# Performance work log

Measured on AMD Instinct MI355X. Metric: run time of the kernel, lower is better.

The kernel has to match this reference:

```python
import jax, jax.numpy as jnp
import numpy as np
from jax import lax

RATIOS = (0.5, 1.0, 2.0)
SCALES = (8, 16, 32)
BASE = 16
STRIDE = 16
N_PRE = 6000
N_POST = 300      # post-NMS proposals kept
NMS_THRESH = 0.7
MIN_SIZE = 16.0


def _anchor_base():
    x = y = BASE / 2.0
    ab = np.zeros((len(RATIOS) * len(SCALES), 4), np.float32)
    for i, r in enumerate(RATIOS):
        for j, s in enumerate(SCALES):
            h = BASE * s * np.sqrt(r)
            w = BASE * s * np.sqrt(1.0 / r)
            k = i * len(SCALES) + j
            ab[k] = [y - h / 2, x - w / 2, y + h / 2, x + w / 2]
    return ab


def _anchors(h, w):
    ab = _anchor_base()
    sy = np.arange(0, h * STRIDE, STRIDE)
    sx = np.arange(0, w * STRIDE, STRIDE)
    sx, sy = np.meshgrid(sx, sy)
    shift = np.stack((sy.ravel(), sx.ravel(), sy.ravel(), sx.ravel()), axis=1)
    # [K, A, 4] -> [K*A, 4], row-major over (y, x) pixels matching NHWC flatten
    return (ab[None, :, :] + shift[:, None, :]).reshape(-1, 4).astype(np.float32)


def _conv(x, w, b, pad):
    y = lax.conv_general_dilated(x, w, (1, 1), ((pad, pad), (pad, pad)),
                                 dimension_numbers=('NCHW', 'OIHW', 'NCHW'))
    return y + b[None, :, None, None]


def _loc2bbox(anchor, loc):
    h = anchor[:, 2] - anchor[:, 0]
    w = anchor[:, 3] - anchor[:, 1]
    cy = anchor[:, 0] + 0.5 * h
    cx = anchor[:, 1] + 0.5 * w
    dy, dx, dh, dw = loc[:, 0], loc[:, 1], loc[:, 2], loc[:, 3]
    ncy = dy * h + cy
    ncx = dx * w + cx
    nh = jnp.exp(dh) * h
    nw = jnp.exp(dw) * w
    return jnp.stack([ncy - 0.5 * nh, ncx - 0.5 * nw, ncy + 0.5 * nh, ncx + 0.5 * nw], axis=1)


def _iou(b):
    tl = jnp.maximum(b[:, None, :2], b[None, :, :2])
    br = jnp.minimum(b[:, None, 2:], b[None, :, 2:])
    wh = jnp.clip(br - tl, 0.0)
    inter = wh[..., 0] * wh[..., 1]
    area = (b[:, 2] - b[:, 0]) * (b[:, 3] - b[:, 1])
    return inter / (area[:, None] + area[None, :] - inter + 1e-9)


def _nms_keep(iou):
    # greedy NMS over score-sorted boxes: suppress later boxes overlapping kept earlier ones
    n = iou.shape[0]
    idx = jnp.arange(n)
    def step(keep, i):
        sup = (iou[i] > NMS_THRESH) & (idx > i) & keep[i]
        return keep & (~sup), None
    keep, _ = lax.scan(step, jnp.ones((n,), dtype=bool), idx)
    return keep


def _proposal(loc, fg, anchor, img_h, img_w, scale=1.0):
    boxes = _loc2bbox(anchor, loc)
    boxes = jnp.stack([jnp.clip(boxes[:, 0], 0.0, img_h),
                       jnp.clip(boxes[:, 1], 0.0, img_w),
                       jnp.clip(boxes[:, 2], 0.0, img_h),
                       jnp.clip(boxes[:, 3], 0.0, img_w)], axis=1)
    hs = boxes[:, 2] - boxes[:, 0]
    ws = boxes[:, 3] - boxes[:, 1]
    ms = MIN_SIZE * scale
    score = jnp.where((hs >= ms) & (ws >= ms), fg, -jnp.inf)
    top, idx = lax.top_k(score, N_PRE)
    bk = boxes[idx]                                    # [N_PRE, 4]
    keep = _nms_keep(_iou(lax.stop_gradient(bk)))      # selection is non-differentiable
    fs = jnp.where(keep, top, -jnp.inf)
    _, o2 = lax.top_k(fs, N_POST)
    return bk[o2]                                      # [N_POST, 4]


def setup_inputs() -> dict:
    key = jax.random.key(0)
    ks = jax.random.split(key, 4)
    C, H, W = 512, 50, 76
    return {
        "feature": jax.random.normal(ks[0], (1, C, H, W), jnp.float32),
        "conv1_w": jax.random.normal(ks[1], (512, C, 3, 3), jnp.float32) * 0.01,
        "conv1_b": jnp.zeros((512,), jnp.float32),
        "score_w": jax.random.normal(ks[2], (18, 512, 1, 1), jnp.float32) * 0.01,
        "score_b": jnp.zeros((18,), jnp.float32),
        "loc_w": jax.random.normal(ks[3], (36, 512, 1, 1), jnp.float32) * 0.01,
        "loc_b": jnp.zeros((36,), jnp.float32),
        "img_h": 800,
        "img_w": 1216,
    }


def reference(feature, conv1_w, conv1_b, score_w, score_b, loc_w, loc_b, img_h, img_w):
    _, c, h, w = feature.shape
    A = 9
    anchor = jnp.asarray(_anchors(h, w))
    x = jax.nn.relu(_conv(feature, conv1_w, conv1_b, 1))
    locs = _conv(x, loc_w, loc_b, 0)
    rpn_locs = locs.transpose(0, 2, 3, 1).reshape(1, -1, 4)
    sc = _conv(x, score_w, score_b, 0).transpose(0, 2, 3, 1)   # [1, h, w, 2A]
    sm = jax.nn.softmax(sc.reshape(1, h, w, A, 2), axis=-1)
    fg = sm[..., 1].reshape(-1)
    rpn_scores = sc.reshape(1, -1, 2)
    rois = _proposal(rpn_locs[0], fg, anchor, float(img_h), float(img_w), scale=1.0)
    return rpn_locs, rpn_scores, rois, anchor
```

## Files before the change

### kernel.cpp

```cpp
#include <hip/hip_runtime.h>

#define HH 50
#define WW2 76
#define NPIX 3800
#define CIN 512
#define NANCH 34200
#define NPRE 6000
#define NPOST 300
#define WPR 94

typedef unsigned long long u64;
typedef unsigned int u32;

__device__ __forceinline__ int PADL(int i) { return i + (i >> 4); }

template <bool DOW>
__global__ __launch_bounds__(256) void rpn_wtrans(const float* __restrict__ wgt,
                                                  float* __restrict__ wt,
                                                  const float* __restrict__ sw,
                                                  const float* __restrict__ lw,
                                                  float* __restrict__ wt2,
                                                  u32* __restrict__ hist,
                                                  u32* __restrict__ info) {
    __shared__ float tile[32][33];
    const int bx = blockIdx.x;
    const int by = blockIdx.y;
    const int t  = threadIdx.x;
    const int tx = t & 31, ty = t >> 5;
    int gid = (by * 144 + bx) * 256 + t;
    if (gid < 65536) hist[gid] = 0u;
    else if (gid < 65552) info[gid - 65536] = 0u;
    if (gid < 32768) {
        int c = gid >> 6, n = gid & 63;
        float v = 0.f;
        if (n < 18) v = sw[n * 512 + c];
        else if (n < 54) v = lw[(n - 18) * 512 + c];
        wt2[((c >> 2) * 64 + n) * 4 + (c & 3)] = v;
    }
    if (!DOW) return;
#pragma unroll
    for (int r = 0; r < 32; r += 8) {
        int ko = by * 32 + ty + r;
        tile[ty + r][tx] = wgt[(size_t)ko * 4608 + bx * 32 + tx];
    }
    __syncthreads();
#pragma unroll
    for (int r = 0; r < 32; r += 8) {
        int cit = bx * 32 + ty + r;
        wt[(size_t)cit * 512 + by * 32 + tx] = tile[tx][ty + r];
    }
}

template <bool USEWT>
__global__ __launch_bounds__(256, 4) void rpn_conv1(
    const float* __restrict__ feat, const float* __restrict__ wsrc,
    float* __restrict__ Xp, int cin_blk) {
    const int yb = blockIdx.x;
    const int kg = blockIdx.y;
    const int cz = blockIdx.z;
    const int t  = threadIdx.x;
    const int kp = t & 31;
    const int ty = t >> 5;
    const int row  = ty >> 2;
    const int xseg = ty & 3;
    const int x0 = xseg * 20;
    __shared__ float in_l[2816];
    __shared__ float w_l[4608];

    const int y0 = yb * 2 - 1;
    int inSrc[11]; u32 inValid = 0, inPad = 0;
#pragma unroll
    for (int k = 0; k < 11; ++k) {
        int q = t + k * 256;
        int c = q / 336, rem = q - c * 336;
        int r = rem / 84, xx = rem - r * 84;
        int gy = y0 + r, gx = xx - 1;
        bool inb = q < 2688;
        bool ok = inb && ((unsigned)gy < 50u) && ((unsigned)gx < 76u);
        inSrc[k] = c * NPIX + gy * 76 + gx;
        if (ok) inValid |= (1u << k);
        else if (inb) inPad |= (1u << k);
    }
#pragma unroll
    for (int k = 0; k < 11; ++k)
        if ((inPad >> k) & 1) in_l[t + k * 256] = 0.f;

    const float* wb;
    int wOffA = 0;
    int wSrc[18];
    if (USEWT) {
        wb = wsrc + (size_t)(cz * cin_blk) * 9 * 512 + kg * 64;
        wOffA = 8 * t - 7 * (t & 63);
    } else {
        wb = wsrc + (size_t)(kg * 64) * 4608 + (size_t)(cz * cin_blk) * 9;
#pragma unroll
        for (int k = 0; k < 18; ++k) {
            int q = t + k * 256;
            int c = q / 576, r2 = q - c * 576;
            int tap = r2 >> 6, ko = r2 & 63;
            wSrc[k] = ko * 4608 + c * 9 + tap;
        }
    }

    const float* fb = feat + (size_t)(cz * cin_blk) * NPIX;
    float acc0[20], acc1[20];
#pragma unroll
    for (int p = 0; p < 20; ++p) { acc0[p] = 0.f; acc1[p] = 0.f; }

    const int niter = cin_blk >> 3;
#pragma unroll 1
    for (int it = 0; it < niter; ++it) {
        __syncthreads();
#pragma unroll
        for (int k = 0; k < 11; ++k)
            if ((inValid >> k) & 1) in_l[t + k * 256] = fb[inSrc[k]];
        if (USEWT) {
#pragma unroll
            for (int k = 0; k < 18; ++k)
                w_l[t + k * 256] = wb[wOffA + k * 2048];
        } else {
#pragma unroll
            for (int k = 0; k < 18; ++k)
                w_l[t + k * 256] = wb[wSrc[k]];
        }
        __syncthreads();
#pragma unroll 1
        for (int c = 0; c < 8; ++c) {
            const float* ir0 = &in_l[(c * 4 + row) * 84 + x0];
            const float* wl  = &w_l[c * 576 + 2 * kp];
#pragma unroll
            for (int r = 0; r < 3; ++r) {
                const float* ir = ir0 + r * 84;
                float win[22];
#pragma unroll
                for (int w = 0; w < 22; ++w) win[w] = ir[w];
                float w00 = wl[(r * 3 + 0) * 64],     w01 = wl[(r * 3 + 1) * 64],     w02 = wl[(r * 3 + 2) * 64];
                float w10 = wl[(r * 3 + 0) * 64 + 1], w11 = wl[(r * 3 + 1) * 64 + 1], w12 = wl[(r * 3 + 2) * 64 + 1];
#pragma unroll
                for (int p = 0; p < 20; ++p) {
                    acc0[p] = fmaf(w00, win[p],     acc0[p]);
                    acc0[p] = fmaf(w01, win[p + 1], acc0[p]);
                    acc0[p] = fmaf(w02, win[p + 2], acc0[p]);
                    acc1[p] = fmaf(w10, win[p],     acc1[p]);
                    acc1[p] = fmaf(w11, win[p + 1], acc1[p]);
                    acc1[p] = fmaf(w12, win[p + 2], acc1[p]);
                }
            }
        }
        fb += 8 * NPIX;
        wb += USEWT ? 8 * 9 * 512 : 72;
    }

    const int k0 = kg * 64 + 2 * kp;
    const int y = yb * 2 + row;
    float* d0 = Xp + ((size_t)cz * 512 + k0) * NPIX + y * 76 + x0;
#pragma unroll
    for (int p = 0; p < 20; p += 2) {
        if (x0 + p + 1 < 76) {
            *reinterpret_cast<float2*>(d0 + p)        = make_float2(acc0[p], acc0[p + 1]);
            *reinterpret_cast<float2*>(d0 + NPIX + p) = make_float2(acc1[p], acc1[p + 1]);
        }
    }
}

__global__ __launch_bounds__(256) void rpn_combine(
    const float* __restrict__ Xp, const float* __restrict__ bias,
    float* __restrict__ Xt, int nz) {
    const int p0 = blockIdx.x * 256;
    const int c0 = blockIdx.y * 16;
    const int t  = threadIdx.x;
    __shared__ float s[16][257];
    const int p = p0 + t;
#pragma unroll 4
    for (int i = 0; i < 16; ++i) {
        float v = 0.f;
        if (p < NPIX) {
            size_t base = (size_t)(c0 + i) * NPIX + p;
            float a = bias[c0 + i];
            for (int z = 0; z < nz; ++z) a += Xp[(size_t)z * 512 * NPIX + base];
            v = fmaxf(a, 0.f);
        }
        s[i][t] = v;
    }
    __syncthreads();
    const int cs = (t & 3) * 4;
    const int pr = t >> 2;
#pragma unroll
    for (int q = 0; q < 4; ++q) {
        int p2 = p0 + pr + q * 64;
        if (p2 < NPIX) {
            int pi = pr + q * 64;
            float4 v = make_float4(s[cs][pi], s[cs + 1][pi], s[cs + 2][pi], s[cs + 3][pi]);
            *reinterpret_cast<float4*>(&Xt[(size_t)p2 * 512 + c0 + cs]) = v;
        }
    }
}

__global__ __launch_bounds__(64) void rpn_head(
    const float* __restrict__ Xt, const float* __restrict__ wt2,
    const float* __restrict__ sb, const float* __restrict__ lb,
    const int* __restrict__ ihp, const int* __restrict__ iwp,
    float* __restrict__ out, float* __restrict__ boxes,
    u32* __restrict__ keys, u32* __restrict__ hist) {
    const int p0 = blockIdx.x * 8;
    const int t  = threadIdx.x;
    __shared__ __align__(16) float xs[8 * 512];
    __shared__ float ovl[8][64];
    const float4* src = reinterpret_cast<const float4*>(Xt + (size_t)p0 * 512);
    float4* dst = reinterpret_cast<float4*>(xs);
#pragma unroll
    for (int i = 0; i < 16; ++i) dst[t + i * 64] = src[t + i * 64];
    __syncthreads();
    float acc[8];
    {
        float b = (t < 18) ? sb[t] : ((t < 54) ? lb[t - 18] : 0.f);
#pragma unroll
        for (int px = 0; px < 8; ++px) acc[px] = b;
    }
    const float4* wv = reinterpret_cast<const float4*>(wt2) + t;
#pragma unroll 4
    for (int c4 = 0; c4 < 128; ++c4) {
        float4 w = wv[c4 * 64];
#pragma unroll
        for (int px = 0; px < 8; ++px) {
            float4 x = *reinterpret_cast<const float4*>(xs + px * 512 + c4 * 4);
            acc[px] = fmaf(w.x, x.x, acc[px]);
            acc[px] = fmaf(w.y, x.y, acc[px]);
            acc[px] = fmaf(w.z, x.z, acc[px]);
            acc[px] = fmaf(w.w, x.w, acc[px]);
        }
    }
#pragma unroll
    for (int px = 0; px < 8; ++px) ovl[px][t] = acc[px];
    __syncthreads();
    const float ch = (float)(*ihp), cw = (float)(*iwp);
#pragma unroll
    for (int pass = 0; pass < 2; ++pass) {
        int a, px;
        bool act;
        if (pass == 0) { act = (t < 63); px = t / 9; a = t - px * 9; }
        else           { act = (t < 9);  px = 7;     a = t; }
        if (act) {
            const int p = p0 + px;
            const float* ov = ovl[px];
            const float s0 = ov[2 * a], s1 = ov[2 * a + 1];
            const float dy = ov[18 + 4 * a], dx = ov[18 + 4 * a + 1];
            const float dh = ov[18 + 4 * a + 2], dw = ov[18 + 4 * a + 3];
            const int yy = p / WW2, xx = p % WW2;
            const int ai = p * 9 + a;
            *reinterpret_cast<float4*>(out + ai * 4) = make_float4(dy, dx, dh, dw);
            *reinterpret_cast<float2*>(out + 136800 + ai * 2) = make_float2(s0, s1);
            double r  = (a < 3) ? 0.5 : (a < 6) ? 1.0 : 2.0;
            int m3 = a % 3;
            double s2 = (m3 == 0) ? 8.0 : (m3 == 1) ? 16.0 : 32.0;
            double hd = (16.0 * s2) * sqrt(r);
            double wd = (16.0 * s2) * sqrt(1.0 / r);
            float ay1 = (float)(8.0 - hd * 0.5), ax1 = (float)(8.0 - wd * 0.5);
            float ay2 = (float)(8.0 + hd * 0.5), ax2 = (float)(8.0 + wd * 0.5);
            float fy = (float)(yy * 16), fx = (float)(xx * 16);
            float A0 = ay1 + fy, A1 = ax1 + fx, A2 = ay2 + fy, A3 = ax2 + fx;
            *reinterpret_cast<float4*>(out + 206400 + ai * 4) = make_float4(A0, A1, A2, A3);
            float ah = __fsub_rn(A2, A0), aw = __fsub_rn(A3, A1);
            float cy = __fadd_rn(A0, __fmul_rn(0.5f, ah));
            float cx = __fadd_rn(A1, __fmul_rn(0.5f, aw));
            float ncy = __fadd_rn(__fmul_rn(dy, ah), cy);
            float ncx = __fadd_rn(__fmul_rn(dx, aw), cx);
            float nh = __fmul_rn(expf(dh), ah);
            float nw = __fmul_rn(expf(dw), aw);
            float b0 = __fsub_rn(ncy, __fmul_rn(0.5f, nh));
            float b1 = __fsub_rn(ncx, __fmul_rn(0.5f, nw));
            float b2 = __fadd_rn(ncy, __fmul_rn(0.5f, nh));
            float b3 = __fadd_rn(ncx, __fmul_rn(0.5f, nw));
            b0 = fminf(fmaxf(b0, 0.f), ch); b2 = fminf(fmaxf(b2, 0.f), ch);
            b1 = fminf(fmaxf(b1, 0.f), cw); b3 = fminf(fmaxf(b3, 0.f), cw);
            float hs = __fsub_rn(b2, b0), wsz = __fsub_rn(b3, b1);
            float m = fmaxf(s0, s1);
            float e0 = expf(__fsub_rn(s0, m)), e1 = expf(__fsub_rn(s1, m));
            float fg = __fdiv_rn(e1, __fadd_rn(e0, e1));
            float score = (hs >= 16.f && wsz >= 16.f) ? fg : -__builtin_inff();
            *reinterpret_cast<float4*>(boxes + ai * 4) = make_float4(b0, b1, b2, b3);
            u32 kb = __float_as_uint(score);
            kb = (kb & 0x80000000u) ? ~kb : (kb | 0x80000000u);
            keys[ai] = kb;
            atomicAdd(&hist[kb >> 16], 1u);
        }
    }
}

__global__ __launch_bounds__(256) void rpn_thresh(const u32* __restrict__ hist,
                                                  u32* __restrict__ info) {
    __shared__ u32 part[256], h2[256];
    __shared__ int segs;
    const int t = threadIdx.x;
    u32 s = 0;
    const u32* hp = hist + t * 256;
    for (int b = 0; b < 256; ++b) s += hp[b];
    part[t] = s;
    __syncthreads();
    for (int off = 1; off < 256; off <<= 1) {
        u32 v = part[t];
        u32 add = (t + off < 256) ? part[t + off] : 0u;
        __syncthreads();
        part[t] = v + add;
        __syncthreads();
    }
    u32 suf  = part[t];
    u32 sufn = (t < 255) ? part[t + 1] : 0u;
    if (suf >= NPRE && sufn < NPRE) segs = t;
    __syncthreads();
    const int seg = segs;
    const u32 above = (seg < 255) ? part[seg + 1] : 0u;
    h2[t] = hist[seg * 256 + t];
    __syncthreads();
    for (int off = 1; off < 256; off <<= 1) {
        u32 v = h2[t];
        u32 add = (t + off < 256) ? h2[t + off] : 0u;
        __syncthreads();
        h2[t] = v + add;
        __syncthreads();
    }
    u32 tot  = above + h2[t];
    u32 totn = above + ((t < 255) ? h2[t + 1] : 0u);
    if (tot >= NPRE && totn < NPRE) info[0] = (u32)(seg * 256 + t);
}

__global__ void rpn_select(const u32* __restrict__ keys, u32* __restrict__ info,
                           u64* __restrict__ selk) {
    const int idx = blockIdx.x * 256 + threadIdx.x;
    const int lane = threadIdx.x & 63;
    u32 k = (idx < NANCH) ? keys[idx] : 0u;
    bool sel = (idx < NANCH) && ((k >> 16) >= info[0]);
    u64 ball = __ballot(sel);
    u32 base = 0;
    if (lane == 0 && ball) base = atomicAdd(&info[2], (u32)__popcll(ball));
    base = __shfl(base, 0);
    if (sel) {
        u32 pos = base + (u32)__popcll(ball & ((1ull << lane) - 1ull));
        if (pos < 8192) selk[pos] = ((u64)k << 32) | (u64)(0xFFFFFFFFu - (u32)idx);
    }
}

__global__ __launch_bounds__(1024) void rpn_sort_local(u64* __restrict__ selk,
                                                       const u32* __restrict__ info) {
    __shared__ u64 s[2176];
    const int t = threadIdx.x;
    const int seg = blockIdx.x;
    const int base = seg * 2048;
    int n = (int)info[2]; if (n > 8192) n = 8192;
    for (int i = t; i < 2048; i += 1024)
        s[PADL(i)] = (base + i < n) ? selk[base + i] : 0ull;
    __syncthreads();
    const bool D = ((seg & 1) == 0);
    for (int k = 2; k <= 2048; k <<= 1) {
        for (int j = k >> 1; j > 0; j >>= 1) {
            int p1 = ((t & ~(j - 1)) << 1) | (t & (j - 1));
            int p2 = p1 | j;
            bool desc = (((p1 & k) == 0) == D);
            u64 A = s[PADL(p1)], B = s[PADL(p2)];
            if (desc ? (A < B) : (A > B)) { s[PADL(p1)] = B; s[PADL(p2)] = A; }
            __syncthreads();
        }
    }
    for (int i = t; i < 2048; i += 1024) selk[base + i] = s[PADL(i)];
}

__global__ __launch_bounds__(512) void rpn_sort_gpass(u64* __restrict__ selk,
                                                      int k, int j) {
    int i = blockIdx.x * 512 + threadIdx.x;
    int p1 = ((i & ~(j - 1)) << 1) | (i & (j - 1));
    int p2 = p1 | j;
    bool desc = ((p1 & k) == 0);
    u64 A = selk[p1], B = selk[p2];
    if (desc ? (A < B) : (A > B)) { selk[p1] = B; selk[p2] = A; }
}

template <bool FINAL>
__global__ __launch_bounds__(1024) void rpn_sort_lmerge(u64* __restrict__ selk, int k,
                                                        const float* __restrict__ boxes,
                                                        float* __restrict__ bk) {
    __shared__ u64 s[2176];
    const int t = threadIdx.x;
    const int base = blockIdx.x * 2048;
    for (int i = t; i < 2048; i += 1024) s[PADL(i)] = selk[base + i];
    __syncthreads();
    const bool desc = ((base & k) == 0);
    for (int j = 1024; j > 0; j >>= 1) {
        int p1 = ((t & ~(j - 1)) << 1) | (t & (j - 1));
        int p2 = p1 | j;
        u64 A = s[PADL(p1)], B = s[PADL(p2)];
        if (desc ? (A < B) : (A > B)) { s[PADL(p1)] = B; s[PADL(p2)] = A; }
        __syncthreads();
    }
    if (FINAL) {
        for (int i = t; i < 2048; i += 1024) {
            int r = base + i;
            if (r < NPRE) {
                u32 oi = 0xFFFFFFFFu - (u32)(s[PADL(i)] & 0xFFFFFFFFull);
                if (oi >= NANCH) oi = 0;
                reinterpret_cast<float4*>(bk)[r] = reinterpret_cast<const float4*>(boxes)[oi];
            }
        }
    } else {
        for (int i = t; i < 2048; i += 1024) selk[base + i] = s[PADL(i)];
    }
}

__global__ __launch_bounds__(64) void rpn_iou(const float* __restrict__ bk,
                                              u64* __restrict__ mask) {
    const int t = threadIdx.x;
    const int bj = blockIdx.x, bi = blockIdx.y;
    const int j0 = bj * 64;
    const int i = bi * 64 + t;
    if (j0 + 63 <= bi * 64) {
        if (i < NPRE) mask[(size_t)i * WPR + bj] = 0ull;
        return;
    }
    __shared__ float4 jb[64];
    jb[t] = (j0 + t < NPRE) ? reinterpret_cast<const float4*>(bk)[j0 + t]
                            : make_float4(0.f, 0.f, 0.f, 0.f);
    __syncthreads();
    if (i >= NPRE) return;
    float4 b = reinterpret_cast<const float4*>(bk)[i];
    float areai = __fmul_rn(__fsub_rn(b.z, b.x), __fsub_rn(b.w, b.y));
    u64 bits = 0ull;
    for (int jj = 0; jj < 64; ++jj) {
        int j = j0 + jj;
        if (j <= i || j >= NPRE) continue;
        float4 c = jb[jj];
        float ty = fmaxf(b.x, c.x), tx = fmaxf(b.y, c.y);
        float by = fminf(b.z, c.z), bx2 = fminf(b.w, c.w);
        float ih = fmaxf(__fsub_rn(by, ty), 0.f);
        float iw = fmaxf(__fsub_rn(bx2, tx), 0.f);
        float inter = __fmul_rn(ih, iw);
        float areaj = __fmul_rn(__fsub_rn(c.z, c.x), __fsub_rn(c.w, c.y));
        float denom = __fadd_rn(__fsub_rn(__fadd_rn(areai, areaj), inter), 1e-9f);
        float iou = __fdiv_rn(inter, denom);
        if (iou > 0.7f) bits |= (1ull << jj);
    }
    mask[(size_t)i * WPR + bj] = bits;
}

__global__ __launch_bounds__(64) void rpn_nms(const u64* __restrict__ mask,
                                              const float* __restrict__ bk,
                                              float* __restrict__ rois) {
    const int lane = threadIdx.x;
    u64 rem0 = 0ull, rem1 = 0ull, curW = 0ull;
    __shared__ unsigned short klist[304];
    int kcnt = 0;
    u64 pm0[16], pm1[16], pmg[16];
#pragma unroll
    for (int u = 0; u < 16; ++u) {
        pm0[u] = mask[(size_t)u * WPR + lane];
        pm1[u] = (lane < 30) ? mask[(size_t)u * WPR + 64 + lane] : 0ull;
        pmg[u] = mask[(size_t)u * WPR + 0];
    }
    bool done = false;
    for (int base = 0; base < NPRE && !done; base += 16) {
        if ((base & 63) == 0) {
            int w = base >> 6;
            curW = (w < 64) ? __shfl(rem0, w) : __shfl(rem1, w - 64);
        }
#pragma unroll
        for (int u = 0; u < 16; ++u) {
            const int i = base + u;
            u64 m0 = pm0[u], m1 = pm1[u], mg = pmg[u];
            const int ni = i + 16;
            pm0[u] = mask[(size_t)ni * WPR + lane];
            pm1[u] = (lane < 30) ? mask[(size_t)ni * WPR + 64 + lane] : 0ull;
            pmg[u] = mask[(size_t)ni * WPR + (ni >> 6)];
            if (((curW >> (i & 63)) & 1ull) == 0ull) {
                rem0 |= m0;
                rem1 |= m1;
                curW |= mg;
                if (lane == 0 && kcnt < 304) klist[kcnt] = (unsigned short)i;
                ++kcnt;
                if (kcnt >= NPOST) { done = true; break; }
            }
        }
    }
    __syncthreads();
    const int nk = kcnt < NPOST ? kcnt : NPOST;
    for (int r = lane; r < nk; r += 64) {
        int bi = klist[r];
        reinterpret_cast<float4*>(rois)[r] = reinterpret_cast<const float4*>(bk)[bi];
    }
    if (kcnt < NPOST) {
        int pos = kcnt;
        for (int i = 0; i < NPRE && pos < NPOST; ++i) {
            int w = i >> 6;
            u64 wv = (w < 64) ? __shfl(rem0, w) : __shfl(rem1, w - 64);
            if ((wv >> (i & 63)) & 1ull) {
                if (lane < 4) rois[pos * 4 + lane] = bk[i * 4 + lane];
                ++pos;
            }
        }
    }
}

extern "C" void kernel_launch(void* const* d_in, const int* in_sizes, int n_in,
                              void* d_out, int out_size, void* d_ws, size_t ws_size,
                              hipStream_t stream) {
    (void)in_sizes; (void)n_in; (void)out_size;
    const float* feat = (const float*)d_in[0];
    const float* w1   = (const float*)d_in[1];
    const float* b1   = (const float*)d_in[2];
    const float* sw   = (const float*)d_in[3];
    const float* sb   = (const float*)d_in[4];
    const float* lw   = (const float*)d_in[5];
    const float* lb   = (const float*)d_in[6];
    const int*   ih   = (const int*)d_in[7];
    const int*   iw   = (const int*)d_in[8];
    float* out = (float*)d_out;

    const size_t WT_B    = 9437184;
    const size_t WT2_B   = 131072;
    const size_t XT_B    = 7782400;
    const size_t REST_B  = WT2_B + 547200 + 136800 + 262144 + 64 + 65536 + 96000 + 4528128;
    const size_t SLICE_B = (size_t)512 * NPIX * 4;
    int nz; bool usewt;
    if      (ws_size >= 8 * SLICE_B + WT_B + XT_B + REST_B) { nz = 8; usewt = true; }
    else if (ws_size >= 4 * SLICE_B + WT_B + XT_B + REST_B) { nz = 4; usewt = true; }
    else if (ws_size >= 2 * SLICE_B + WT_B + XT_B + REST_B) { nz = 2; usewt = true; }
    else                                                    { nz = 2; usewt = false; }

    char* p = (char*)d_ws;
    float* Xp = (float*)p;           p += (size_t)nz * SLICE_B;
    float* wt = nullptr;
    if (usewt) { wt = (float*)p;     p += WT_B; }
    float* Xt     = (float*)p;       p += XT_B;
    float* wt2    = (float*)p;       p += WT2_B;
    float* boxes  = (float*)p;       p += 547200;
    u32*   keys   = (u32*)p;         p += 136800;
    u32*   hist   = (u32*)p;         p += 262144;
    u32*   info   = (u32*)p;         p += 64;
    u64*   selk   = (u64*)p;         p += 65536;
    float* bk     = (float*)p;       p += 96000;
    u64*   mask   = (u64*)p;

    const int cin_blk = 512 / nz;

    if (usewt) {
        rpn_wtrans<true><<<dim3(144, 16), 256, 0, stream>>>(w1, wt, sw, lw, wt2, hist, info);
        rpn_conv1<true><<<dim3(25, 8, nz), 256, 0, stream>>>(feat, wt, Xp, cin_blk);
    } else {
        rpn_wtrans<false><<<dim3(144, 16), 256, 0, stream>>>(w1, nullptr, sw, lw, wt2, hist, info);
        rpn_conv1<false><<<dim3(25, 8, nz), 256, 0, stream>>>(feat, w1, Xp, cin_blk);
    }
    rpn_combine<<<dim3(15, 32), 256, 0, stream>>>(Xp, b1, Xt, nz);
    rpn_head<<<475, 64, 0, stream>>>(Xt, wt2, sb, lb, ih, iw, out, boxes, keys, hist);
    rpn_thresh<<<1, 256, 0, stream>>>(hist, info);
    rpn_select<<<(NANCH + 255) / 256, 256, 0, stream>>>(keys, info, selk);
    rpn_sort_local<<<4, 1024, 0, stream>>>(selk, info);
    rpn_sort_gpass<<<8, 512, 0, stream>>>(selk, 4096, 2048);
    rpn_sort_lmerge<false><<<4, 1024, 0, stream>>>(selk, 4096, nullptr, nullptr);
    rpn_sort_gpass<<<8, 512, 0, stream>>>(selk, 8192, 4096);
    rpn_sort_gpass<<<8, 512, 0, stream>>>(selk, 8192, 2048);
    rpn_sort_lmerge<true><<<4, 1024, 0, stream>>>(selk, 8192, boxes, bk);
    rpn_iou<<<dim3(WPR, WPR), 64, 0, stream>>>(bk, mask);
    rpn_nms<<<1, 64, 0, stream>>>(mask, bk, out + 205200);
}
```

Baseline: 611.5 us.

## Fuse threshold with selection and merge sort passes into one kernel

Merges the histogram-threshold kernel and the compaction kernel into a single 1024-thread block that finds the threshold and then loops over all keys to compact them. It also replaces the chain of global bitonic passes and local merge kernels with one 1024-thread block that does the final two merge levels in 64 KB of shared memory and gathers the boxes. This cuts the number of kernel launches from eight to three on this short tail. In exchange, the compaction and merge now each run on a single workgroup instead of many.

```diff
diff --git a/kernel.cpp b/kernel.cpp
--- a/kernel.cpp
+++ b/kernel.cpp
@@ -287,56 +287,69 @@
     }
 }
 
-__global__ __launch_bounds__(256) void rpn_thresh(const u32* __restrict__ hist,
-                                                  u32* __restrict__ info) {
+__global__ __launch_bounds__(1024) void rpn_threshsel(const u32* __restrict__ hist,
+                                                      u32* __restrict__ info,
+                                                      const u32* __restrict__ keys,
+                                                      u64* __restrict__ selk) {
+    __shared__ u32 tmp[1024];
     __shared__ u32 part[256], h2[256];
     __shared__ int segs;
+    __shared__ u32 Tsh;
     const int t = threadIdx.x;
-    u32 s = 0;
-    const u32* hp = hist + t * 256;
-    for (int b = 0; b < 256; ++b) s += hp[b];
-    part[t] = s;
+    {
+        u32 s = 0;
+        const u32* hp = hist + t * 64;
+#pragma unroll 8
+        for (int b = 0; b < 64; ++b) s += hp[b];
+        tmp[t] = s;
+    }
+    __syncthreads();
+    if (t < 256) part[t] = tmp[4 * t] + tmp[4 * t + 1] + tmp[4 * t + 2] + tmp[4 * t + 3];
     __syncthreads();
     for (int off = 1; off < 256; off <<= 1) {
-        u32 v = part[t];
-        u32 add = (t + off < 256) ? part[t + off] : 0u;
-        __syncthreads();
-        part[t] = v + add;
-        __syncthreads();
-    }
-    u32 suf  = part[t];
-    u32 sufn = (t < 255) ? part[t + 1] : 0u;
-    if (suf >= NPRE && sufn < NPRE) segs = t;
+        u32 v = 0, add = 0;
+        if (t < 256) { v = part[t]; add = (t + off < 256) ? part[t + off] : 0u; }
+        __syncthreads();
+        if (t < 256) part[t] = v + add;
+        __syncthreads();
+    }
+    if (t < 256) {
+        u32 suf  = part[t];
+        u32 sufn = (t < 255) ? part[t + 1] : 0u;
+        if (suf >= NPRE && sufn < NPRE) segs = t;
+    }
     __syncthreads();
     const int seg = segs;
     const u32 above = (seg < 255) ? part[seg + 1] : 0u;
-    h2[t] = hist[seg * 256 + t];
+    if (t < 256) h2[t] = hist[seg * 256 + t];
     __syncthreads();
     for (int off = 1; off < 256; off <<= 1) {
-        u32 v = h2[t];
-        u32 add = (t + off < 256) ? h2[t + off] : 0u;
-        __syncthreads();
-        h2[t] = v + add;
-        __syncthreads();
-    }
-    u32 tot  = above + h2[t];
-    u32 totn = above + ((t < 255) ? h2[t + 1] : 0u);
-    if (tot >= NPRE && totn < NPRE) info[0] = (u32)(seg * 256 + t);
-}
-
-__global__ void rpn_select(const u32* __restrict__ keys, u32* __restrict__ info,
-                           u64* __restrict__ selk) {
-    const int idx = blockIdx.x * 256 + threadIdx.x;
-    const int lane = threadIdx.x & 63;
-    u32 k = (idx < NANCH) ? keys[idx] : 0u;
-    bool sel = (idx < NANCH) && ((k >> 16) >= info[0]);
-    u64 ball = __ballot(sel);
-    u32 base = 0;
-    if (lane == 0 && ball) base = atomicAdd(&info[2], (u32)__popcll(ball));
-    base = __shfl(base, 0);
-    if (sel) {
-        u32 pos = base + (u32)__popcll(ball & ((1ull << lane) - 1ull));
-        if (pos < 8192) selk[pos] = ((u64)k << 32) | (u64)(0xFFFFFFFFu - (u32)idx);
+        u32 v = 0, add = 0;
+        if (t < 256) { v = h2[t]; add = (t + off < 256) ? h2[t + off] : 0u; }
+        __syncthreads();
+        if (t < 256) h2[t] = v + add;
+        __syncthreads();
+    }
+    if (t < 256) {
+        u32 tot  = above + h2[t];
+        u32 totn = above + ((t < 255) ? h2[t + 1] : 0u);
+        if (tot >= NPRE && totn < NPRE) Tsh = (u32)(seg * 256 + t);
+    }
+    __syncthreads();
+    const u32 T = Tsh;
+    const int lane = t & 63;
+    for (int base = 0; base < NANCH; base += 1024) {
+        int idx = base + t;
+        u32 k = (idx < NANCH) ? keys[idx] : 0u;
+        bool sel = (idx < NANCH) && ((k >> 16) >= T);
+        u64 ball = __ballot(sel);
+        u32 wbase = 0;
+        if (lane == 0 && ball) wbase = atomicAdd(&info[2], (u32)__popcll(ball));
+        wbase = __shfl(wbase, 0);
+        if (sel) {
+            u32 pos = wbase + (u32)__popcll(ball & ((1ull << lane) - 1ull));
+            if (pos < 8192) selk[pos] = ((u64)k << 32) | (u64)(0xFFFFFFFFu - (u32)idx);
+        }
     }
 }
 
@@ -364,44 +377,40 @@
     for (int i = t; i < 2048; i += 1024) selk[base + i] = s[PADL(i)];
 }
 
-__global__ __launch_bounds__(512) void rpn_sort_gpass(u64* __restrict__ selk,
-                                                      int k, int j) {
-    int i = blockIdx.x * 512 + threadIdx.x;
-    int p1 = ((i & ~(j - 1)) << 1) | (i & (j - 1));
-    int p2 = p1 | j;
-    bool desc = ((p1 & k) == 0);
-    u64 A = selk[p1], B = selk[p2];
-    if (desc ? (A < B) : (A > B)) { selk[p1] = B; selk[p2] = A; }
-}
-
-template <bool FINAL>
-__global__ __launch_bounds__(1024) void rpn_sort_lmerge(u64* __restrict__ selk, int k,
-                                                        const float* __restrict__ boxes,
-                                                        float* __restrict__ bk) {
-    __shared__ u64 s[2176];
+__global__ __launch_bounds__(1024) void rpn_sort_merge(const u64* __restrict__ selk,
+                                                       const float* __restrict__ boxes,
+                                                       float* __restrict__ bk) {
+    __shared__ u64 s[8192];
     const int t = threadIdx.x;
-    const int base = blockIdx.x * 2048;
-    for (int i = t; i < 2048; i += 1024) s[PADL(i)] = selk[base + i];
-    __syncthreads();
-    const bool desc = ((base & k) == 0);
-    for (int j = 1024; j > 0; j >>= 1) {
-        int p1 = ((t & ~(j - 1)) << 1) | (t & (j - 1));
-        int p2 = p1 | j;
-        u64 A = s[PADL(p1)], B = s[PADL(p2)];
-        if (desc ? (A < B) : (A > B)) { s[PADL(p1)] = B; s[PADL(p2)] = A; }
-        __syncthreads();
-    }
-    if (FINAL) {
-        for (int i = t; i < 2048; i += 1024) {
-            int r = base + i;
-            if (r < NPRE) {
-                u32 oi = 0xFFFFFFFFu - (u32)(s[PADL(i)] & 0xFFFFFFFFull);
-                if (oi >= NANCH) oi = 0;
-                reinterpret_cast<float4*>(bk)[r] = reinterpret_cast<const float4*>(boxes)[oi];
-            }
-        }
-    } else {
-        for (int i = t; i < 2048; i += 1024) selk[base + i] = s[PADL(i)];
+    for (int i = t; i < 8192; i += 1024) s[i] = selk[i];
+    __syncthreads();
+    for (int j = 2048; j > 0; j >>= 1) {
+#pragma unroll 4
+        for (int z = 0; z < 4; ++z) {
+            int pi = t + z * 1024;
+            int p1 = ((pi & ~(j - 1)) << 1) | (pi & (j - 1));
+            int p2 = p1 | j;
+            bool desc = ((p1 & 4096) == 0);
+            u64 A = s[p1], B = s[p2];
+            if (desc ? (A < B) : (A > B)) { s[p1] = B; s[p2] = A; }
+        }
+        __syncthreads();
+    }
+    for (int j = 4096; j > 0; j >>= 1) {
+#pragma unroll 4
+        for (int z = 0; z < 4; ++z) {
+            int pi = t + z * 1024;
+            int p1 = ((pi & ~(j - 1)) << 1) | (pi & (j - 1));
+            int p2 = p1 | j;
+            u64 A = s[p1], B = s[p2];
+            if (A < B) { s[p1] = B; s[p2] = A; }
+        }
+        __syncthreads();
+    }
+    for (int i = t; i < NPRE; i += 1024) {
+        u32 oi = 0xFFFFFFFFu - (u32)(s[i] & 0xFFFFFFFFull);
+        if (oi >= NANCH) oi = 0;
+        reinterpret_cast<float4*>(bk)[i] = reinterpret_cast<const float4*>(boxes)[oi];
     }
 }
 
@@ -548,14 +557,9 @@
     }
     rpn_combine<<<dim3(15, 32), 256, 0, stream>>>(Xp, b1, Xt, nz);
     rpn_head<<<475, 64, 0, stream>>>(Xt, wt2, sb, lb, ih, iw, out, boxes, keys, hist);
-    rpn_thresh<<<1, 256, 0, stream>>>(hist, info);
-    rpn_select<<<(NANCH + 255) / 256, 256, 0, stream>>>(keys, info, selk);
+    rpn_threshsel<<<1, 1024, 0, stream>>>(hist, info, keys, selk);
     rpn_sort_local<<<4, 1024, 0, stream>>>(selk, info);
-    rpn_sort_gpass<<<8, 512, 0, stream>>>(selk, 4096, 2048);
-    rpn_sort_lmerge<false><<<4, 1024, 0, stream>>>(selk, 4096, nullptr, nullptr);
-    rpn_sort_gpass<<<8, 512, 0, stream>>>(selk, 8192, 4096);
-    rpn_sort_gpass<<<8, 512, 0, stream>>>(selk, 8192, 2048);
-    rpn_sort_lmerge<true><<<4, 1024, 0, stream>>>(selk, 8192, boxes, bk);
+    rpn_sort_merge<<<1, 1024, 0, stream>>>(selk, boxes, bk);
     rpn_iou<<<dim3(WPR, WPR), 64, 0, stream>>>(bk, mask);
     rpn_nms<<<1, 64, 0, stream>>>(mask, bk, out + 205200);
 }
```

Result: slower. 640.0 us (+4.7%).
